# Performance work log

Measured on AMD Instinct MI355X. Metric: run time of the kernel, lower is better.

## Reference

```python
import jax, jax.numpy as jnp
import numpy as np

B, T, V, E, U = 1024, 128, 32000, 128, 512


def setup_inputs() -> dict:
    key = jax.random.key(0)
    ks = jax.random.split(key, 8)
    s = lambda k, *sh: jax.random.normal(k, sh, dtype=jnp.float32) * 0.05
    return {
        "tokens": jax.random.randint(ks[0], (B, T), 0, V, dtype=jnp.int32),
        "emb": s(ks[1], V, E),
        "Wx0": s(ks[2], E, U),
        "Wh0": s(ks[3], U, U),
        "b0": jnp.zeros((U,), jnp.float32),
        "Wx1": s(ks[4], U, U),
        "Wh1": s(ks[5], U, U),
        "b1": jnp.zeros((U,), jnp.float32),
        "Wo": s(ks[6], U, 1),
        "bo": jnp.zeros((1,), jnp.float32),
    }


def reference(tokens, emb, Wx0, Wh0, b0, Wx1, Wh1, b1, Wo, bo):
    # Embedding lookup: [B, T, E]
    x = emb[tokens]
    xs = jnp.swapaxes(x, 0, 1)  # [T, B, E] for time-major scan
    h0 = jnp.zeros((tokens.shape[0], Wh0.shape[0]), x.dtype)
    h1 = jnp.zeros((tokens.shape[0], Wh1.shape[0]), x.dtype)

    def step(carry, xt):
        h0, h1 = carry
        # SimpleRNNCell layer 0: h' = tanh(x@Wx + h@Wh + b)
        h0 = jnp.tanh(xt @ Wx0 + h0 @ Wh0 + b0)
        # SimpleRNNCell layer 1 stacked on out0
        h1 = jnp.tanh(h0 @ Wx1 + h1 @ Wh1 + b1)
        return (h0, h1), None

    (h0, h1), _ = jax.lax.scan(step, (h0, h1), xs)
    logits = h1 @ Wo + bo            # [B, 1]
    return jax.nn.sigmoid(logits)
```

## Files before the change

### kernel.cpp

```cpp
#include <hip/hip_runtime.h>
#include <hip/hip_bf16.h>

#define B_ 1024
#define T_ 128
#define E_ 128
#define U_ 512
#define V_ 32000
#define NC 16
#define NG 16
#define MB 64
#define NB 32

#define CTR_OFF 0
#define XMASK_OFF (512u << 10)
#define H0H_OFF (1u << 20)
#define H0L_OFF (3u << 20)
#define H1H_OFF (5u << 20)
#define H1L_OFF (7u << 20)
#define EMBW_OFF (9u << 20)
#define ZERO_BYTES (9u << 20)

typedef unsigned int uint32;
typedef __bf16 bf16x8 __attribute__((ext_vector_type(8)));
typedef float f32x4 __attribute__((ext_vector_type(4)));
typedef unsigned short us8 __attribute__((ext_vector_type(8)));

__device__ __forceinline__ unsigned short f2b(float f) {
  uint32 u = __builtin_bit_cast(uint32, f);
  u += 0x7fffu + ((u >> 16) & 1u);
  return (unsigned short)(u >> 16);
}
__device__ __forceinline__ float b2f(unsigned short h) {
  return __builtin_bit_cast(float, (uint32)h << 16);
}

__device__ __forceinline__ bf16x8 lds_frag(const unsigned short* s, int row, int k, int K) {
  uint32 off = (uint32)((row * K + k) * 2) ^ (uint32)((row & 7) << 4);
  us8 v = *(const us8*)((const char*)s + off);
  return __builtin_bit_cast(bf16x8, v);
}
__device__ __forceinline__ bf16x8 g_frag(const unsigned short* p) {
  us8 v = *(const us8*)p;
  return __builtin_bit_cast(bf16x8, v);
}
__device__ __forceinline__ void st_coh(unsigned short* p, unsigned short v) {
  __hip_atomic_store(p, v, __ATOMIC_RELAXED, __HIP_MEMORY_SCOPE_AGENT);
}
template <bool FAST>
__device__ __forceinline__ void st_h(unsigned short* p, unsigned short v) {
  if (FAST) *p = v; else st_coh(p, v);
}

__device__ __forceinline__ void bar_core(uint32* ctr, int phase, int g, int tid,
                                         bool fence, bool l1inv) {
  asm volatile("s_waitcnt vmcnt(0)" ::: "memory");
  __syncthreads();
  if (tid == 0) {
    uint32* a = &ctr[(uint32)((phase << 4) | g) << 4];
    __hip_atomic_fetch_add(a, 1u, __ATOMIC_RELAXED, __HIP_MEMORY_SCOPE_AGENT);
    while (__hip_atomic_load(a, __ATOMIC_RELAXED, __HIP_MEMORY_SCOPE_AGENT) < NC)
      __builtin_amdgcn_s_sleep(1);
    if (fence) __builtin_amdgcn_fence(__ATOMIC_ACQUIRE, "agent");
    if (l1inv) asm volatile("buffer_inv" ::: "memory");
  }
  __syncthreads();
}

__global__ void rnn_init(unsigned char* ws) {
  const uint4 z = {0u, 0u, 0u, 0u};
  uint4* p = (uint4*)ws;
  size_t n = ZERO_BYTES / 16;
  for (size_t j = (size_t)blockIdx.x * blockDim.x + threadIdx.x; j < n;
       j += (size_t)gridDim.x * blockDim.x)
    p[j] = z;
}

__global__ __launch_bounds__(256) void embw_gemm(const float* __restrict__ emb,
                                                 const float* __restrict__ Wx0,
                                                 unsigned short* __restrict__ embW) {
  const int tid = threadIdx.x;
  const int lane = tid & 63;
  const int wv = tid >> 6;
  const int arow = lane & 15;
  const int kgrp = (lane >> 4) * 8;
  const int vrow = blockIdx.x * 64 + wv * 16;

  bf16x8 a[4];
  for (int kt = 0; kt < 4; ++kt) {
    const float* p = emb + (size_t)(vrow + arow) * E_ + kt * 32 + kgrp;
    float4 f0 = ((const float4*)p)[0];
    float4 f1 = ((const float4*)p)[1];
    us8 u;
    u[0] = f2b(f0.x); u[1] = f2b(f0.y); u[2] = f2b(f0.z); u[3] = f2b(f0.w);
    u[4] = f2b(f1.x); u[5] = f2b(f1.y); u[6] = f2b(f1.z); u[7] = f2b(f1.w);
    a[kt] = __builtin_bit_cast(bf16x8, u);
  }
  const int c0 = blockIdx.y * 64;
  for (int nt = 0; nt < 4; ++nt) {
    const int col = c0 + nt * 16 + (lane & 15);
    f32x4 acc = {0.f, 0.f, 0.f, 0.f};
    for (int kt = 0; kt < 4; ++kt) {
      us8 ub;
      for (int j = 0; j < 8; ++j)
        ub[j] = f2b(Wx0[(size_t)(kt * 32 + kgrp + j) * U_ + col]);
      acc = __builtin_amdgcn_mfma_f32_16x16x32_bf16(a[kt], __builtin_bit_cast(bf16x8, ub),
                                                    acc, 0, 0, 0);
    }
    const int crow = vrow + (lane >> 4) * 4;
    for (int i = 0; i < 4; ++i)
      embW[(size_t)(crow + i) * U_ + col] = f2b(acc[i]);
  }
}

template <bool FAST>
__device__ __forceinline__ void rnn_loop(
    const int* __restrict__ tokens, const unsigned short* __restrict__ embW,
    unsigned short* h0h, unsigned short* h0l, unsigned short* h1h,
    unsigned short* h1l, uint32* ctr, const unsigned short* sWh0h,
    const unsigned short* sWh0l, const unsigned short* sWx1h,
    const unsigned short* sWh1h, const unsigned short* sWh1l, int g, int tid,
    int r0, int c0, int colL, int rowB, int kgrp, int rowA, float b0v, float b1v) {
  unsigned short embPre[4];
  for (int i = 0; i < 4; ++i) {
    int tk = tokens[(size_t)(r0 + rowB + i) * T_ + 0];
    embPre[i] = embW[(size_t)tk * U_ + c0 + colL];
  }

  for (int t = 0; t <= T_; ++t) {
    const size_t rb0 = (size_t)((t & 1) ^ 1) * (B_ * U_);

    bf16x8 h0h_r[16], h0l_r[16];
    {
      const unsigned short* aph = h0h + rb0 + (size_t)rowA * U_ + kgrp;
      const unsigned short* apl = h0l + rb0 + (size_t)rowA * U_ + kgrp;
#pragma unroll
      for (int kt = 0; kt < 16; ++kt) {
        h0h_r[kt] = g_frag(aph + kt * 32);
        h0l_r[kt] = g_frag(apl + kt * 32);
      }
    }

    if (t >= 1) {
      const size_t rb1 = (size_t)(t & 1) * (B_ * U_);
      const size_t wb1 = (size_t)((t - 1) & 1) * (B_ * U_);
      f32x4 acc = {b1v, b1v, b1v, b1v};
      const unsigned short* a1h = h1h + rb1 + (size_t)rowA * U_ + kgrp;
      const unsigned short* a1l = h1l + rb1 + (size_t)rowA * U_ + kgrp;
#pragma unroll
      for (int kt = 0; kt < 16; ++kt) {
        bf16x8 ah = g_frag(a1h + kt * 32);
        bf16x8 al = g_frag(a1l + kt * 32);
        bf16x8 bxh = lds_frag(sWx1h, colL, kt * 32 + kgrp, U_);
        bf16x8 bh = lds_frag(sWh1h, colL, kt * 32 + kgrp, U_);
        acc = __builtin_amdgcn_mfma_f32_16x16x32_bf16(h0h_r[kt], bxh, acc, 0, 0, 0);
        acc = __builtin_amdgcn_mfma_f32_16x16x32_bf16(h0l_r[kt], bxh, acc, 0, 0, 0);
        acc = __builtin_amdgcn_mfma_f32_16x16x32_bf16(ah, bh, acc, 0, 0, 0);
        acc = __builtin_amdgcn_mfma_f32_16x16x32_bf16(al, bh, acc, 0, 0, 0);
        if (kt < 15) {
          bf16x8 bl = lds_frag(sWh1l, colL, kt * 32 + kgrp, 480);
          acc = __builtin_amdgcn_mfma_f32_16x16x32_bf16(ah, bl, acc, 0, 0, 0);
        }
      }
      size_t ob = wb1 + (size_t)(r0 + rowB) * U_ + (c0 + colL);
      for (int i = 0; i < 4; ++i) {
        float v = tanhf(acc[i]);
        unsigned short hi = f2b(v);
        st_h<FAST>(&h1h[ob + (size_t)i * U_], hi);
        st_h<FAST>(&h1l[ob + (size_t)i * U_], f2b(v - b2f(hi)));
      }
    }

    if (t < T_) {
      const size_t wbuf = (size_t)(t & 1) * (B_ * U_);
      f32x4 acc;
      for (int i = 0; i < 4; ++i) acc[i] = b0v + b2f(embPre[i]);
#pragma unroll
      for (int kt = 0; kt < 16; ++kt) {
        bf16x8 bh = lds_frag(sWh0h, colL, kt * 32 + kgrp, U_);
        bf16x8 bl = lds_frag(sWh0l, colL, kt * 32 + kgrp, U_);
        acc = __builtin_amdgcn_mfma_f32_16x16x32_bf16(h0h_r[kt], bh, acc, 0, 0, 0);
        acc = __builtin_amdgcn_mfma_f32_16x16x32_bf16(h0l_r[kt], bh, acc, 0, 0, 0);
        acc = __builtin_amdgcn_mfma_f32_16x16x32_bf16(h0h_r[kt], bl, acc, 0, 0, 0);
      }
      size_t ob = wbuf + (size_t)(r0 + rowB) * U_ + (c0 + colL);
      for (int i = 0; i < 4; ++i) {
        float v = tanhf(acc[i]);
        unsigned short hi = f2b(v);
        st_h<FAST>(&h0h[ob + (size_t)i * U_], hi);
        st_h<FAST>(&h0l[ob + (size_t)i * U_], f2b(v - b2f(hi)));
      }

      if (t + 1 < T_) {
        for (int i = 0; i < 4; ++i) {
          int tk = tokens[(size_t)(r0 + rowB + i) * T_ + (t + 1)];
          embPre[i] = embW[(size_t)tk * U_ + c0 + colL];
        }
      }
      bar_core(ctr, t, g, tid, !FAST, FAST);
    }
  }
}

__global__ __launch_bounds__(512, 2) void rnn_main(
    const int* __restrict__ tokens, const float* __restrict__ b0,
    const float* __restrict__ Wh0, const float* __restrict__ Wx1,
    const float* __restrict__ Wh1, const float* __restrict__ b1,
    unsigned char* ws) {
  __shared__ unsigned short sWh0h[NB * U_];
  __shared__ unsigned short sWh0l[NB * U_];
  __shared__ unsigned short sWx1h[NB * U_];
  __shared__ unsigned short sWh1h[NB * U_];
  __shared__ unsigned short sWh1l[NB * 480];
  __shared__ uint32 sFast;

  const int tid = threadIdx.x;
  const int bid = blockIdx.x;
  const int g = bid & (NG - 1);
  const int c = bid >> 4;
  const int r0 = g * MB;
  const int c0 = c * NB;

  uint32* ctr = (uint32*)(ws + CTR_OFF);
  unsigned short* h0h = (unsigned short*)(ws + H0H_OFF);
  unsigned short* h0l = (unsigned short*)(ws + H0L_OFF);
  unsigned short* h1h = (unsigned short*)(ws + H1H_OFF);
  unsigned short* h1l = (unsigned short*)(ws + H1L_OFF);
  const unsigned short* embW = (const unsigned short*)(ws + EMBW_OFF);

  for (int idx = tid; idx < NB * U_; idx += 512) {
    int cl = idx & 31, k = idx >> 5;
    float v = Wh0[(size_t)k * U_ + c0 + cl];
    unsigned short hi = f2b(v);
    uint32 off = (uint32)((cl * U_ + k) * 2) ^ (uint32)((cl & 7) << 4);
    *(unsigned short*)((char*)sWh0h + off) = hi;
    *(unsigned short*)((char*)sWh0l + off) = f2b(v - b2f(hi));
  }
  for (int idx = tid; idx < NB * U_; idx += 512) {
    int cl = idx & 31, k = idx >> 5;
    float v = Wx1[(size_t)k * U_ + c0 + cl];
    uint32 off = (uint32)((cl * U_ + k) * 2) ^ (uint32)((cl & 7) << 4);
    *(unsigned short*)((char*)sWx1h + off) = f2b(v);
  }
  for (int idx = tid; idx < NB * U_; idx += 512) {
    int cl = idx & 31, k = idx >> 5;
    float v = Wh1[(size_t)k * U_ + c0 + cl];
    unsigned short hi = f2b(v);
    uint32 off = (uint32)((cl * U_ + k) * 2) ^ (uint32)((cl & 7) << 4);
    *(unsigned short*)((char*)sWh1h + off) = hi;
    if (k < 480) {
      uint32 offl = (uint32)((cl * 480 + k) * 2) ^ (uint32)((cl & 7) << 4);
      *(unsigned short*)((char*)sWh1l + offl) = f2b(v - b2f(hi));
    }
  }

  {
    uint32 xcd;
    asm volatile("s_getreg_b32 %0, hwreg(HW_REG_XCC_ID)" : "=s"(xcd));
    uint32* xm = (uint32*)(ws + XMASK_OFF) + (uint32)g * 16;
    if (tid == 0)
      __hip_atomic_fetch_or(xm, 1u << (xcd & 31u), __ATOMIC_RELAXED,
                            __HIP_MEMORY_SCOPE_AGENT);
    bar_core(ctr, T_, g, tid, true, false);
    if (tid == 0) {
      uint32 m = __hip_atomic_load(xm, __ATOMIC_RELAXED, __HIP_MEMORY_SCOPE_AGENT);
      sFast = (__popc(m) == 1) ? 1u : 0u;
    }
  }

  const int lane = tid & 63;
  const int wv = tid >> 6;
  const int mt = wv >> 1;
  const int nt = wv & 1;
  const int colL = nt * 16 + (lane & 15);
  const int rowB = mt * 16 + ((lane >> 4) << 2);
  const int kgrp = (lane >> 4) * 8;
  const int rowA = r0 + mt * 16 + (lane & 15);
  const float b0v = b0[c0 + colL];
  const float b1v = b1[c0 + colL];

  __syncthreads();
  const bool fast = (sFast != 0);

  if (fast)
    rnn_loop<true>(tokens, embW, h0h, h0l, h1h, h1l, ctr, sWh0h, sWh0l, sWx1h,
                   sWh1h, sWh1l, g, tid, r0, c0, colL, rowB, kgrp, rowA, b0v, b1v);
  else
    rnn_loop<false>(tokens, embW, h0h, h0l, h1h, h1l, ctr, sWh0h, sWh0l, sWx1h,
                    sWh1h, sWh1l, g, tid, r0, c0, colL, rowB, kgrp, rowA, b0v, b1v);
}

__global__ void rnn_final(const unsigned short* __restrict__ h1h,
                          const unsigned short* __restrict__ h1l,
                          const float* __restrict__ Wo,
                          const float* __restrict__ bo, float* __restrict__ out) {
  int lane = threadIdx.x & 63;
  int b = blockIdx.x * 4 + (threadIdx.x >> 6);
  us8 hh = *(const us8*)(h1h + (size_t)b * U_ + lane * 8);
  us8 hl = *(const us8*)(h1l + (size_t)b * U_ + lane * 8);
  const float4* wp = (const float4*)(Wo + lane * 8);
  float4 w0 = wp[0], w1 = wp[1];
  float s = (b2f(hh[0]) + b2f(hl[0])) * w0.x + (b2f(hh[1]) + b2f(hl[1])) * w0.y +
            (b2f(hh[2]) + b2f(hl[2])) * w0.z + (b2f(hh[3]) + b2f(hl[3])) * w0.w +
            (b2f(hh[4]) + b2f(hl[4])) * w1.x + (b2f(hh[5]) + b2f(hl[5])) * w1.y +
            (b2f(hh[6]) + b2f(hl[6])) * w1.z + (b2f(hh[7]) + b2f(hl[7])) * w1.w;
  for (int off = 32; off > 0; off >>= 1) s += __shfl_down(s, off, 64);
  if (lane == 0) out[b] = 1.0f / (1.0f + expf(-(s + bo[0])));
}

extern "C" void kernel_launch(void* const* d_in, const int* in_sizes, int n_in,
                              void* d_out, int out_size, void* d_ws, size_t ws_size,
                              hipStream_t stream) {
  const int* tokens = (const int*)d_in[0];
  const float* emb = (const float*)d_in[1];
  const float* Wx0 = (const float*)d_in[2];
  const float* Wh0 = (const float*)d_in[3];
  const float* b0 = (const float*)d_in[4];
  const float* Wx1 = (const float*)d_in[5];
  const float* Wh1 = (const float*)d_in[6];
  const float* b1 = (const float*)d_in[7];
  const float* Wo = (const float*)d_in[8];
  const float* bo = (const float*)d_in[9];
  unsigned char* ws = (unsigned char*)d_ws;
  float* out = (float*)d_out;

  hipLaunchKernelGGL(rnn_init, dim3(1024), dim3(256), 0, stream, ws);
  hipLaunchKernelGGL(embw_gemm, dim3(V_ / 64, U_ / 64), dim3(256), 0, stream,
                     emb, Wx0, (unsigned short*)(ws + EMBW_OFF));
  hipLaunchKernelGGL(rnn_main, dim3(NC * NG), dim3(512), 0, stream, tokens,
                     b0, Wh0, Wx1, Wh1, b1, ws);
  hipLaunchKernelGGL(rnn_final, dim3(256), dim3(256), 0, stream,
                     (const unsigned short*)(ws + H1H_OFF) + (size_t)1 * B_ * U_,
                     (const unsigned short*)(ws + H1L_OFF) + (size_t)1 * B_ * U_,
                     Wo, bo, out);
}
```

Before: 2.225 ms.

## Replace per-step group barriers with per-wave flag signalling and split accumulators

Drops the block-wide atomic counter barrier at each timestep. Each wave now publishes progress flags and waits only on the 16 column-blocks that produce its own row slice, which allows finer-grained overlap between blocks. Blocks shrink to 256 threads, with each wave covering both 16-column tiles. Accumulators are split into independent chains to expose more MFMA parallelism, and embedding and h1 loads are hoisted ahead of compute. The risk is extra flag polling traffic, cache invalidation cost, and higher register pressure from holding all h1 fragments.

New measurement: 2.384 ms. +7.1%, slower.

```diff
diff --git a/kernel.cpp b/kernel.cpp
--- a/kernel.cpp
+++ b/kernel.cpp
@@ -10,9 +10,12 @@
 #define NG 16
 #define MB 64
 #define NB 32
+#define HS ((size_t)B_ * U_)
 
 #define CTR_OFF 0
 #define XMASK_OFF (512u << 10)
+#define FH0_OFF (520u << 10)
+#define FH1_OFF (528u << 10)
 #define H0H_OFF (1u << 20)
 #define H0L_OFF (3u << 20)
 #define H1H_OFF (5u << 20)
@@ -25,6 +28,8 @@
 typedef float f32x4 __attribute__((ext_vector_type(4)));
 typedef unsigned short us8 __attribute__((ext_vector_type(8)));
 
+#define MFMA __builtin_amdgcn_mfma_f32_16x16x32_bf16
+
 __device__ __forceinline__ unsigned short f2b(float f) {
   uint32 u = __builtin_bit_cast(uint32, f);
   u += 0x7fffu + ((u >> 16) & 1u);
@@ -51,8 +56,34 @@
   if (FAST) *p = v; else st_coh(p, v);
 }
 
-__device__ __forceinline__ void bar_core(uint32* ctr, int phase, int g, int tid,
-                                         bool fence, bool l1inv) {
+template <bool FAST>
+__device__ __forceinline__ void wave_signal(uint32* f, uint32 val, int lane) {
+  asm volatile("s_waitcnt vmcnt(0)" ::: "memory");
+  if (lane == 0) {
+    if (FAST) *(volatile uint32*)f = val;
+    else __hip_atomic_store(f, val, __ATOMIC_RELAXED, __HIP_MEMORY_SCOPE_AGENT);
+  }
+}
+
+template <bool FAST>
+__device__ __forceinline__ void wave_wait(const uint32* f0, const uint32* f1,
+                                          int t, int lane) {
+  if (t == 0) return;
+  const uint32 tgt = (lane < 16) ? (uint32)t : ((lane < 32) ? (uint32)(t - 1) : 0u);
+  const uint32* p = (lane < 16) ? (f0 + lane) : (f1 + (lane & 15));
+  while (true) {
+    uint32 v;
+    if (FAST) v = *(const volatile uint32*)p;
+    else v = __hip_atomic_load(p, __ATOMIC_RELAXED, __HIP_MEMORY_SCOPE_AGENT);
+    if (__all(v >= tgt)) break;
+    if (FAST) asm volatile("buffer_inv" ::: "memory");
+    __builtin_amdgcn_s_sleep(2);
+  }
+  if (FAST) asm volatile("buffer_inv\n\ts_waitcnt vmcnt(0)" ::: "memory");
+  else __builtin_amdgcn_fence(__ATOMIC_ACQUIRE, "agent");
+}
+
+__device__ __forceinline__ void bar_agent(uint32* ctr, int phase, int g, int tid) {
   asm volatile("s_waitcnt vmcnt(0)" ::: "memory");
   __syncthreads();
   if (tid == 0) {
@@ -60,8 +91,7 @@
     __hip_atomic_fetch_add(a, 1u, __ATOMIC_RELAXED, __HIP_MEMORY_SCOPE_AGENT);
     while (__hip_atomic_load(a, __ATOMIC_RELAXED, __HIP_MEMORY_SCOPE_AGENT) < NC)
       __builtin_amdgcn_s_sleep(1);
-    if (fence) __builtin_amdgcn_fence(__ATOMIC_ACQUIRE, "agent");
-    if (l1inv) asm volatile("buffer_inv" ::: "memory");
+    __builtin_amdgcn_fence(__ATOMIC_ACQUIRE, "agent");
   }
   __syncthreads();
 }
@@ -103,8 +133,7 @@
       us8 ub;
       for (int j = 0; j < 8; ++j)
         ub[j] = f2b(Wx0[(size_t)(kt * 32 + kgrp + j) * U_ + col]);
-      acc = __builtin_amdgcn_mfma_f32_16x16x32_bf16(a[kt], __builtin_bit_cast(bf16x8, ub),
-                                                    acc, 0, 0, 0);
+      acc = MFMA(a[kt], __builtin_bit_cast(bf16x8, ub), acc, 0, 0, 0);
     }
     const int crow = vrow + (lane >> 4) * 4;
     for (int i = 0; i < 4; ++i)
@@ -116,19 +145,27 @@
 __device__ __forceinline__ void rnn_loop(
     const int* __restrict__ tokens, const unsigned short* __restrict__ embW,
     unsigned short* h0h, unsigned short* h0l, unsigned short* h1h,
-    unsigned short* h1l, uint32* ctr, const unsigned short* sWh0h,
-    const unsigned short* sWh0l, const unsigned short* sWx1h,
-    const unsigned short* sWh1h, const unsigned short* sWh1l, int g, int tid,
-    int r0, int c0, int colL, int rowB, int kgrp, int rowA, float b0v, float b1v) {
-  unsigned short embPre[4];
-  for (int i = 0; i < 4; ++i) {
-    int tk = tokens[(size_t)(r0 + rowB + i) * T_ + 0];
-    embPre[i] = embW[(size_t)tk * U_ + c0 + colL];
-  }
+    unsigned short* h1l, const uint32* f0w, const uint32* f1w, uint32* myF0,
+    uint32* myF1, const unsigned short* sWh0h, const unsigned short* sWh0l,
+    const unsigned short* sWx1h, const unsigned short* sWh1h,
+    const unsigned short* sWh1l, int r0, int c0, int lane, int rowB, int kgrp,
+    int rowA, float b0v0, float b0v1, float b1v0, float b1v1) {
+  const int l15 = lane & 15;
+  const float b0a[2] = {b0v0, b0v1};
+  const float b1a[2] = {b1v0, b1v1};
+
+  unsigned short embP[2][4];
+#pragma unroll
+  for (int nt = 0; nt < 2; ++nt)
+    for (int i = 0; i < 4; ++i) {
+      int tk = tokens[(size_t)(r0 + rowB + i) * T_ + 0];
+      embP[nt][i] = embW[(size_t)tk * U_ + c0 + nt * 16 + l15];
+    }
 
   for (int t = 0; t <= T_; ++t) {
-    const size_t rb0 = (size_t)((t & 1) ^ 1) * (B_ * U_);
-
+    wave_wait<FAST>(f0w, f1w, t, lane);
+
+    const size_t rb0 = (size_t)((t & 1) ^ 1) * HS;
     bf16x8 h0h_r[16], h0l_r[16];
     {
       const unsigned short* aph = h0h + rb0 + (size_t)rowA * U_ + kgrp;
@@ -139,69 +176,93 @@
         h0l_r[kt] = g_frag(apl + kt * 32);
       }
     }
-
+    bf16x8 a1h_r[16], a1l_r[16];
     if (t >= 1) {
-      const size_t rb1 = (size_t)(t & 1) * (B_ * U_);
-      const size_t wb1 = (size_t)((t - 1) & 1) * (B_ * U_);
-      f32x4 acc = {b1v, b1v, b1v, b1v};
+      const size_t rb1 = (size_t)(t & 1) * HS;
       const unsigned short* a1h = h1h + rb1 + (size_t)rowA * U_ + kgrp;
       const unsigned short* a1l = h1l + rb1 + (size_t)rowA * U_ + kgrp;
 #pragma unroll
       for (int kt = 0; kt < 16; ++kt) {
-        bf16x8 ah = g_frag(a1h + kt * 32);
-        bf16x8 al = g_frag(a1l + kt * 32);
-        bf16x8 bxh = lds_frag(sWx1h, colL, kt * 32 + kgrp, U_);
-        bf16x8 bh = lds_frag(sWh1h, colL, kt * 32 + kgrp, U_);
-        acc = __builtin_amdgcn_mfma_f32_16x16x32_bf16(h0h_r[kt], bxh, acc, 0, 0, 0);
-        acc = __builtin_amdgcn_mfma_f32_16x16x32_bf16(h0l_r[kt], bxh, acc, 0, 0, 0);
-        acc = __builtin_amdgcn_mfma_f32_16x16x32_bf16(ah, bh, acc, 0, 0, 0);
-        acc = __builtin_amdgcn_mfma_f32_16x16x32_bf16(al, bh, acc, 0, 0, 0);
-        if (kt < 15) {
-          bf16x8 bl = lds_frag(sWh1l, colL, kt * 32 + kgrp, 480);
-          acc = __builtin_amdgcn_mfma_f32_16x16x32_bf16(ah, bl, acc, 0, 0, 0);
+        a1h_r[kt] = g_frag(a1h + kt * 32);
+        a1l_r[kt] = g_frag(a1l + kt * 32);
+      }
+    }
+    unsigned short embN[2][4];
+    if (t + 1 < T_) {
+#pragma unroll
+      for (int nt = 0; nt < 2; ++nt)
+        for (int i = 0; i < 4; ++i) {
+          int tk = tokens[(size_t)(r0 + rowB + i) * T_ + (t + 1)];
+          embN[nt][i] = embW[(size_t)tk * U_ + c0 + nt * 16 + l15];
+        }
+    }
+
+    if (t < T_) {
+      const size_t wbuf = (size_t)(t & 1) * HS;
+#pragma unroll
+      for (int nt = 0; nt < 2; ++nt) {
+        const int colL = nt * 16 + l15;
+        f32x4 aC, aD = {0.f, 0.f, 0.f, 0.f};
+        for (int i = 0; i < 4; ++i) aC[i] = b0a[nt] + b2f(embP[nt][i]);
+#pragma unroll
+        for (int kt = 0; kt < 16; ++kt) {
+          bf16x8 bh = lds_frag(sWh0h, colL, kt * 32 + kgrp, U_);
+          bf16x8 bl = lds_frag(sWh0l, colL, kt * 32 + kgrp, U_);
+          aC = MFMA(h0h_r[kt], bh, aC, 0, 0, 0);
+          aD = MFMA(h0l_r[kt], bh, aD, 0, 0, 0);
+          aD = MFMA(h0h_r[kt], bl, aD, 0, 0, 0);
+        }
+        size_t ob = wbuf + (size_t)(r0 + rowB) * U_ + (c0 + colL);
+        for (int i = 0; i < 4; ++i) {
+          float v = tanhf(aC[i] + aD[i]);
+          unsigned short hi = f2b(v);
+          st_h<FAST>(&h0h[ob + (size_t)i * U_], hi);
+          st_h<FAST>(&h0l[ob + (size_t)i * U_], f2b(v - b2f(hi)));
         }
       }
-      size_t ob = wb1 + (size_t)(r0 + rowB) * U_ + (c0 + colL);
-      for (int i = 0; i < 4; ++i) {
-        float v = tanhf(acc[i]);
-        unsigned short hi = f2b(v);
-        st_h<FAST>(&h1h[ob + (size_t)i * U_], hi);
-        st_h<FAST>(&h1l[ob + (size_t)i * U_], f2b(v - b2f(hi)));
-      }
-    }
-
-    if (t < T_) {
-      const size_t wbuf = (size_t)(t & 1) * (B_ * U_);
-      f32x4 acc;
-      for (int i = 0; i < 4; ++i) acc[i] = b0v + b2f(embPre[i]);
-#pragma unroll
-      for (int kt = 0; kt < 16; ++kt) {
-        bf16x8 bh = lds_frag(sWh0h, colL, kt * 32 + kgrp, U_);
-        bf16x8 bl = lds_frag(sWh0l, colL, kt * 32 + kgrp, U_);
-        acc = __builtin_amdgcn_mfma_f32_16x16x32_bf16(h0h_r[kt], bh, acc, 0, 0, 0);
-        acc = __builtin_amdgcn_mfma_f32_16x16x32_bf16(h0l_r[kt], bh, acc, 0, 0, 0);
-        acc = __builtin_amdgcn_mfma_f32_16x16x32_bf16(h0h_r[kt], bl, acc, 0, 0, 0);
-      }
-      size_t ob = wbuf + (size_t)(r0 + rowB) * U_ + (c0 + colL);
-      for (int i = 0; i < 4; ++i) {
-        float v = tanhf(acc[i]);
-        unsigned short hi = f2b(v);
-        st_h<FAST>(&h0h[ob + (size_t)i * U_], hi);
-        st_h<FAST>(&h0l[ob + (size_t)i * U_], f2b(v - b2f(hi)));
-      }
-
-      if (t + 1 < T_) {
+      wave_signal<FAST>(myF0, (uint32)(t + 1), lane);
+    }
+
+    if (t >= 1) {
+      const size_t wb1 = (size_t)((t - 1) & 1) * HS;
+#pragma unroll
+      for (int nt = 0; nt < 2; ++nt) {
+        const int colL = nt * 16 + l15;
+        f32x4 aA = {0.f, 0.f, 0.f, 0.f};
+        f32x4 aB = {b1a[nt], b1a[nt], b1a[nt], b1a[nt]};
+#pragma unroll
+        for (int kt = 0; kt < 16; ++kt) {
+          bf16x8 bxh = lds_frag(sWx1h, colL, kt * 32 + kgrp, U_);
+          aA = MFMA(h0h_r[kt], bxh, aA, 0, 0, 0);
+          aA = MFMA(h0l_r[kt], bxh, aA, 0, 0, 0);
+          bf16x8 bh = lds_frag(sWh1h, colL, kt * 32 + kgrp, U_);
+          aB = MFMA(a1h_r[kt], bh, aB, 0, 0, 0);
+          aB = MFMA(a1l_r[kt], bh, aB, 0, 0, 0);
+          if (kt < 15) {
+            bf16x8 bl = lds_frag(sWh1l, colL, kt * 32 + kgrp, 480);
+            aB = MFMA(a1h_r[kt], bl, aB, 0, 0, 0);
+          }
+        }
+        size_t ob = wb1 + (size_t)(r0 + rowB) * U_ + (c0 + colL);
         for (int i = 0; i < 4; ++i) {
-          int tk = tokens[(size_t)(r0 + rowB + i) * T_ + (t + 1)];
-          embPre[i] = embW[(size_t)tk * U_ + c0 + colL];
+          float v = tanhf(aA[i] + aB[i]);
+          unsigned short hi = f2b(v);
+          st_h<FAST>(&h1h[ob + (size_t)i * U_], hi);
+          st_h<FAST>(&h1l[ob + (size_t)i * U_], f2b(v - b2f(hi)));
         }
       }
-      bar_core(ctr, t, g, tid, !FAST, FAST);
-    }
-  }
-}
-
-__global__ __launch_bounds__(512, 2) void rnn_main(
+      wave_signal<FAST>(myF1, (uint32)t, lane);
+    }
+
+    if (t + 1 < T_) {
+#pragma unroll
+      for (int nt = 0; nt < 2; ++nt)
+        for (int i = 0; i < 4; ++i) embP[nt][i] = embN[nt][i];
+    }
+  }
+}
+
+__global__ __launch_bounds__(256, 1) void rnn_main(
     const int* __restrict__ tokens, const float* __restrict__ b0,
     const float* __restrict__ Wh0, const float* __restrict__ Wx1,
     const float* __restrict__ Wh1, const float* __restrict__ b1,
@@ -221,13 +282,15 @@
   const int c0 = c * NB;
 
   uint32* ctr = (uint32*)(ws + CTR_OFF);
+  uint32* fH0 = (uint32*)(ws + FH0_OFF);
+  uint32* fH1 = (uint32*)(ws + FH1_OFF);
   unsigned short* h0h = (unsigned short*)(ws + H0H_OFF);
   unsigned short* h0l = (unsigned short*)(ws + H0L_OFF);
   unsigned short* h1h = (unsigned short*)(ws + H1H_OFF);
   unsigned short* h1l = (unsigned short*)(ws + H1L_OFF);
   const unsigned short* embW = (const unsigned short*)(ws + EMBW_OFF);
 
-  for (int idx = tid; idx < NB * U_; idx += 512) {
+  for (int idx = tid; idx < NB * U_; idx += 256) {
     int cl = idx & 31, k = idx >> 5;
     float v = Wh0[(size_t)k * U_ + c0 + cl];
     unsigned short hi = f2b(v);
@@ -235,13 +298,13 @@
     *(unsigned short*)((char*)sWh0h + off) = hi;
     *(unsigned short*)((char*)sWh0l + off) = f2b(v - b2f(hi));
   }
-  for (int idx = tid; idx < NB * U_; idx += 512) {
+  for (int idx = tid; idx < NB * U_; idx += 256) {
     int cl = idx & 31, k = idx >> 5;
     float v = Wx1[(size_t)k * U_ + c0 + cl];
     uint32 off = (uint32)((cl * U_ + k) * 2) ^ (uint32)((cl & 7) << 4);
     *(unsigned short*)((char*)sWx1h + off) = f2b(v);
   }
-  for (int idx = tid; idx < NB * U_; idx += 512) {
+  for (int idx = tid; idx < NB * U_; idx += 256) {
     int cl = idx & 31, k = idx >> 5;
     float v = Wh1[(size_t)k * U_ + c0 + cl];
     unsigned short hi = f2b(v);
@@ -260,7 +323,7 @@
     if (tid == 0)
       __hip_atomic_fetch_or(xm, 1u << (xcd & 31u), __ATOMIC_RELAXED,
                             __HIP_MEMORY_SCOPE_AGENT);
-    bar_core(ctr, T_, g, tid, true, false);
+    bar_agent(ctr, T_, g, tid);
     if (tid == 0) {
       uint32 m = __hip_atomic_load(xm, __ATOMIC_RELAXED, __HIP_MEMORY_SCOPE_AGENT);
       sFast = (__popc(m) == 1) ? 1u : 0u;
@@ -268,25 +331,30 @@
   }
 
   const int lane = tid & 63;
-  const int wv = tid >> 6;
-  const int mt = wv >> 1;
-  const int nt = wv & 1;
-  const int colL = nt * 16 + (lane & 15);
+  const int mt = tid >> 6;
+  const int l15 = lane & 15;
   const int rowB = mt * 16 + ((lane >> 4) << 2);
   const int kgrp = (lane >> 4) * 8;
-  const int rowA = r0 + mt * 16 + (lane & 15);
-  const float b0v = b0[c0 + colL];
-  const float b1v = b1[c0 + colL];
+  const int rowA = r0 + mt * 16 + l15;
+  const float b0v0 = b0[c0 + l15], b0v1 = b0[c0 + 16 + l15];
+  const float b1v0 = b1[c0 + l15], b1v1 = b1[c0 + 16 + l15];
+
+  const uint32* f0w = fH0 + (((uint32)g * 4 + mt) << 4);
+  const uint32* f1w = fH1 + (((uint32)g * 4 + mt) << 4);
+  uint32* myF0 = (uint32*)f0w + c;
+  uint32* myF1 = (uint32*)f1w + c;
 
   __syncthreads();
   const bool fast = (sFast != 0);
 
   if (fast)
-    rnn_loop<true>(tokens, embW, h0h, h0l, h1h, h1l, ctr, sWh0h, sWh0l, sWx1h,
-                   sWh1h, sWh1l, g, tid, r0, c0, colL, rowB, kgrp, rowA, b0v, b1v);
+    rnn_loop<true>(tokens, embW, h0h, h0l, h1h, h1l, f0w, f1w, myF0, myF1,
+                   sWh0h, sWh0l, sWx1h, sWh1h, sWh1l, r0, c0, lane, rowB, kgrp,
+                   rowA, b0v0, b0v1, b1v0, b1v1);
   else
-    rnn_loop<false>(tokens, embW, h0h, h0l, h1h, h1l, ctr, sWh0h, sWh0l, sWx1h,
-                    sWh1h, sWh1l, g, tid, r0, c0, colL, rowB, kgrp, rowA, b0v, b1v);
+    rnn_loop<false>(tokens, embW, h0h, h0l, h1h, h1l, f0w, f1w, myF0, myF1,
+                    sWh0h, sWh0l, sWx1h, sWh1h, sWh1l, r0, c0, lane, rowB, kgrp,
+                    rowA, b0v0, b0v1, b1v0, b1v1);
 }
 
 __global__ void rnn_final(const unsigned short* __restrict__ h1h,
@@ -326,7 +394,7 @@
   hipLaunchKernelGGL(rnn_init, dim3(1024), dim3(256), 0, stream, ws);
   hipLaunchKernelGGL(embw_gemm, dim3(V_ / 64, U_ / 64), dim3(256), 0, stream,
                      emb, Wx0, (unsigned short*)(ws + EMBW_OFF));
-  hipLaunchKernelGGL(rnn_main, dim3(NC * NG), dim3(512), 0, stream, tokens,
+  hipLaunchKernelGGL(rnn_main, dim3(NC * NG), dim3(256), 0, stream, tokens,
                      b0, Wh0, Wx1, Wh1, b1, ws);
   hipLaunchKernelGGL(rnn_final, dim3(256), dim3(256), 0, stream,
                      (const unsigned short*)(ws + H1H_OFF) + (size_t)1 * B_ * U_,
```
